# Optimization experiments

Hardware: AMD Instinct MI355X
Metric: run time of the kernel (lower is better)

The kernel has to match this reference:

```python
import jax, jax.numpy as jnp
import numpy as np

D_MODEL = 1024
D_STATE = 64


def setup_inputs() -> dict:
    key = jax.random.key(0)
    k_x, k_a, k_b, k_c, k_d = jax.random.split(key, 5)
    x = jax.random.normal(k_x, (4, 4096, D_MODEL), dtype=jnp.float32)
    # parameter init mirrors _init_parameters
    A_diag = jax.random.uniform(k_a, (D_STATE,), minval=-0.5, maxval=0.5, dtype=jnp.float32)
    def xavier(k, shape):
        fan_in, fan_out = shape
        limit = float(np.sqrt(6.0 / (fan_in + fan_out)))
        return jax.random.uniform(k, shape, minval=-limit, maxval=limit, dtype=jnp.float32)
    B = xavier(k_b, (D_MODEL, D_STATE))
    C = xavier(k_c, (D_STATE, D_MODEL))
    D = xavier(k_d, (D_MODEL, D_MODEL)) * 0.1
    return {"x": x, "A_diag": A_diag, "B": B, "C": C, "D": D}


def reference(x, A_diag, B, C, D):
    # h_t = sigmoid(A_diag) * h_{t-1} + x_t @ B ; y_t = h_t @ C + x_t @ D
    # dropout is identity in eval mode.
    a = jax.nn.sigmoid(A_diag)                      # [S_state]
    u = jnp.einsum('btd,ds->bts', x, B)             # precompute input drive [B,T,S]

    def step(h, u_t):                               # h: [B,S], u_t: [B,S]
        h = a * h + u_t
        return h, h

    h0 = jnp.zeros((x.shape[0], A_diag.shape[0]), dtype=x.dtype)
    _, hs = jax.lax.scan(step, h0, jnp.swapaxes(u, 0, 1))  # hs: [T,B,S]
    hs = jnp.swapaxes(hs, 0, 1)                            # [B,T,S]
    y = jnp.einsum('bts,sd->btd', hs, C) + jnp.einsum('btd,de->bte', x, D)
    return y
```

## Files before the change

kernel.cpp:

```cpp
#include <hip/hip_runtime.h>
#include <hip/hip_bf16.h>

using bf16x8 = __attribute__((ext_vector_type(8))) __bf16;
using f32x4  = __attribute__((ext_vector_type(4))) float;
using f32x16 = __attribute__((ext_vector_type(16))) float;

#define MTOT   16384
#define DMODEL 1024
#define DSTATE 64
#define KBIG   1088

__device__ __forceinline__ ushort f2b(float f) {
  __hip_bfloat16 h = __float2bfloat16(f);
  return *reinterpret_cast<ushort*>(&h);
}

__device__ __forceinline__ void gld_lds16(const ushort* g, const char* l) {
  using gptr_t = const __attribute__((address_space(1))) uint32_t*;
  using lptr_t = __attribute__((address_space(3))) uint32_t*;
  __builtin_amdgcn_global_load_lds(
      reinterpret_cast<gptr_t>(reinterpret_cast<uintptr_t>(g)),
      reinterpret_cast<lptr_t>(static_cast<uint32_t>(reinterpret_cast<uintptr_t>(l))),
      16, 0, 0);
}

#define BARRIER() do { asm volatile("" ::: "memory"); __builtin_amdgcn_s_barrier(); asm volatile("" ::: "memory"); } while (0)
#define VMCNT8() asm volatile("s_waitcnt vmcnt(8)" ::: "memory")
#define VMCNT0() asm volatile("s_waitcnt vmcnt(0)" ::: "memory")

__global__ void prep_params(const float* __restrict__ A_diag, const float* __restrict__ B,
                            const float* __restrict__ C, const float* __restrict__ D,
                            ushort* __restrict__ Wt, ushort* __restrict__ Btu,
                            float* __restrict__ aSig) {
  int i = blockIdx.x * blockDim.x + threadIdx.x;
  int stride = gridDim.x * blockDim.x;
  for (int idx = i; idx < DMODEL * KBIG; idx += stride) {
    int n = idx / KBIG, k = idx % KBIG;
    float v = (k < DSTATE) ? C[k * DMODEL + n] : D[(size_t)(k - DSTATE) * DMODEL + n];
    Wt[idx] = f2b(v);
  }
  for (int idx = i; idx < DSTATE * DMODEL; idx += stride) {
    int s = idx >> 10, k = idx & 1023;
    Btu[idx] = f2b(B[k * DSTATE + s]);
  }
  if (i < DSTATE) aSig[i] = 1.0f / (1.0f + expf(-A_diag[i]));
}

__global__ __launch_bounds__(256) void fused_xu(const float* __restrict__ x,
    const ushort* __restrict__ Btu, const float* __restrict__ aSig,
    ushort* __restrict__ Z, float* __restrict__ Uloc, float* __restrict__ carry) {
  __shared__ ushort As[64][136];
  __shared__ float  Ul[64][68];
  int tid = threadIdx.x;
  int w = tid >> 6, lane = tid & 63;
  int l16 = lane & 15, lh = lane >> 4;
  int row0 = blockIdx.x * 64;

  f32x4 acc[4] = {};
  float4 xv[4][2];
#pragma unroll
  for (int p = 0; p < 4; ++p) {
    int fi = p * 256 + tid;
    int r = fi >> 4, kq = fi & 15;
    const float* src = x + (size_t)(row0 + r) * 1024 + kq * 8;
    xv[p][0] = *reinterpret_cast<const float4*>(src);
    xv[p][1] = *reinterpret_cast<const float4*>(src + 4);
  }
  for (int c = 0; c < 8; ++c) {
    int k0 = c * 128;
#pragma unroll
    for (int p = 0; p < 4; ++p) {
      int fi = p * 256 + tid;
      int r = fi >> 4, kq = fi & 15;
      ushort o[8] = {f2b(xv[p][0].x), f2b(xv[p][0].y), f2b(xv[p][0].z), f2b(xv[p][0].w),
                     f2b(xv[p][1].x), f2b(xv[p][1].y), f2b(xv[p][1].z), f2b(xv[p][1].w)};
      uint4 pk = *reinterpret_cast<uint4*>(o);
      *reinterpret_cast<uint4*>(&Z[(size_t)(row0 + r) * KBIG + DSTATE + k0 + kq * 8]) = pk;
      *reinterpret_cast<uint4*>(&As[r][kq * 8]) = pk;
    }
    __syncthreads();
    if (c < 7) {
      int k1 = k0 + 128;
#pragma unroll
      for (int p = 0; p < 4; ++p) {
        int fi = p * 256 + tid;
        int r = fi >> 4, kq = fi & 15;
        const float* src = x + (size_t)(row0 + r) * 1024 + k1 + kq * 8;
        xv[p][0] = *reinterpret_cast<const float4*>(src);
        xv[p][1] = *reinterpret_cast<const float4*>(src + 4);
      }
    }
#pragma unroll
    for (int ks = 0; ks < 4; ++ks) {
      bf16x8 af = *reinterpret_cast<const bf16x8*>(&As[w * 16 + l16][ks * 32 + lh * 8]);
#pragma unroll
      for (int n = 0; n < 4; ++n) {
        bf16x8 bf = *reinterpret_cast<const bf16x8*>(
            &Btu[(size_t)(n * 16 + l16) * 1024 + k0 + ks * 32 + lh * 8]);
        acc[n] = __builtin_amdgcn_mfma_f32_16x16x32_bf16(af, bf, acc[n], 0, 0, 0);
      }
    }
    __syncthreads();
  }
#pragma unroll
  for (int n = 0; n < 4; ++n)
#pragma unroll
    for (int j = 0; j < 4; ++j)
      Ul[w * 16 + lh * 4 + j][n * 16 + l16] = acc[n][j];
  __syncthreads();
  int s = lane;
  float as = aSig[s];
  float h = 0.0f;
  int g = blockIdx.x * 4 + w;
#pragma unroll
  for (int i = 0; i < 16; ++i) {
    h = fmaf(as, h, Ul[w * 16 + i][s]);
    Uloc[(size_t)(g * 16 + i) * 64 + s] = h;
  }
  carry[(size_t)g * 64 + s] = h;
}

__global__ __launch_bounds__(256) void scan_fix2(const float* __restrict__ aSig,
    const float* __restrict__ Uloc, const float* __restrict__ carry,
    ushort* __restrict__ Z) {
  int w = threadIdx.x >> 6, s = threadIdx.x & 63;
  int g = blockIdx.x * 4 + w;
  int b = g >> 8, c = g & 255;
  float as = aSig[s];
  float aL = as;
#pragma unroll
  for (int q = 0; q < 4; ++q) aL *= aL;
  const float* cb = carry + ((size_t)b << 8) * 64 + s;
  float H = 0.0f;
  for (int c0 = 0; c0 < 256; c0 += 16) {
    if (c0 >= c) break;
    float v[16];
#pragma unroll
    for (int i = 0; i < 16; ++i) v[i] = cb[(size_t)(c0 + i) * 64];
#pragma unroll
    for (int i = 0; i < 16; ++i)
      if (c0 + i < c) H = fmaf(aL, H, v[i]);
  }
  float p = as;
  size_t ubase = (size_t)g * 16 * 64 + s;
  size_t zbase = (size_t)(g * 16) * KBIG + s;
#pragma unroll
  for (int i = 0; i < 16; ++i) {
    float h = fmaf(p, H, Uloc[ubase + (size_t)i * 64]);
    p *= as;
    Z[zbase + (size_t)i * KBIG] = f2b(h);
  }
}

__global__ __launch_bounds__(512) void gemm256(const ushort* __restrict__ A, int lda,
                                               const ushort* __restrict__ Bt, int ldb,
                                               float* __restrict__ Cc, int ldc, int K) {
  extern __shared__ __align__(128) char smem[];
  const int tid = threadIdx.x;
  const int wid = tid >> 6, lane = tid & 63;
  const int wm = wid >> 2, wn = wid & 3;
  const int l32 = lane & 31, kh = lane >> 5;

  int bid = blockIdx.x;
  int swz = (bid & 7) * ((int)gridDim.x >> 3) + (bid >> 3);
  const int bmRow = (swz >> 2) * 256;
  const int bnCol = (swz & 3) * 256;
  const int NT = K / 64;

  const int sRow = lane >> 3;
  const int sCol = (((lane & 7) ^ (lane >> 3)) << 3);

  const ushort* aBase = A + (size_t)(bmRow + wid * 8 + sRow) * lda + sCol;
  const ushort* bBase = Bt + (size_t)(bnCol + wid * 8 + sRow) * ldb + sCol;
  char* aDst0 = smem + (wid * 8) * 128;
  char* bDst0 = smem + 32768 + (wid * 8) * 128;

  const int aRB = (wm * 128 + l32) * 128 + ((kh ^ (l32 & 7)) << 4);
  const int bRB = 32768 + (wn * 64 + l32) * 128 + ((kh ^ (l32 & 7)) << 4);

  f32x16 acc[4][2] = {};
  bf16x8 aC[4], bC[2], aN[4], bN[2];

  auto stageA = [&](int buf, int t, int h) {
    const ushort* g0 = aBase + (size_t)(h * 128) * lda + (size_t)t * 64;
    const char* d = aDst0 + buf + h * 128 * 128;
    gld_lds16(g0, d);
    gld_lds16(g0 + (size_t)64 * lda, d + 64 * 128);
  };
  auto stageB = [&](int buf, int t, int h) {
    const ushort* g0 = bBase + (size_t)(h * 128) * ldb + (size_t)t * 64;
    const char* d = bDst0 + buf + h * 128 * 128;
    gld_lds16(g0, d);
    gld_lds16(g0 + (size_t)64 * ldb, d + 64 * 128);
  };
  auto readA = [&](bf16x8 (&d)[4], int buf, int ks) {
#pragma unroll
    for (int mb = 0; mb < 4; ++mb)
      d[mb] = *reinterpret_cast<const bf16x8*>(smem + buf + ((aRB + mb * 4096) ^ (ks << 5)));
  };
  auto readB = [&](bf16x8 (&d)[2], int buf, int ks) {
#pragma unroll
    for (int qn = 0; qn < 2; ++qn)
      d[qn] = *reinterpret_cast<const bf16x8*>(smem + buf + ((bRB + qn * 4096) ^ (ks << 5)));
  };
  auto mfmaC = [&](bf16x8 (&a4)[4], bf16x8 (&b2)[2]) {
    __builtin_amdgcn_s_setprio(1);
#pragma unroll
    for (int mb = 0; mb < 4; ++mb)
#pragma unroll
      for (int qn = 0; qn < 2; ++qn)
        acc[mb][qn] = __builtin_amdgcn_mfma_f32_32x32x16_bf16(
            a4[mb], b2[qn], acc[mb][qn], 0, 0, 0);
    __builtin_amdgcn_s_setprio(0);
  };

  stageA(0, 0, 0); stageA(0, 0, 1); stageB(0, 0, 0); stageB(0, 0, 1);
  stageA(65536, 1, 0); stageA(65536, 1, 1); stageB(65536, 1, 0); stageB(65536, 1, 1);
  VMCNT8();
  BARRIER();
  readA(aC, 0, 0); readB(bC, 0, 0);

  for (int t = 0; t < NT; ++t) {
    const int buf = (t & 1) << 16;
    const bool st2 = (t + 2 < NT);
    const bool nxt = (t + 1 < NT);
    readA(aN, buf, 1); readB(bN, buf, 1);
    mfmaC(aC, bC);
    readA(aC, buf, 2); readB(bC, buf, 2);
    mfmaC(aN, bN);
    readA(aN, buf, 3); readB(bN, buf, 3);
    mfmaC(aC, bC);
    BARRIER();
    if (st2) {
      stageA(buf, t + 2, 0); stageA(buf, t + 2, 1);
      stageB(buf, t + 2, 0); stageB(buf, t + 2, 1);
      VMCNT8();
    } else {
      VMCNT0();
    }
    BARRIER();
    if (nxt) { readA(aC, buf ^ 65536, 0); readB(bC, buf ^ 65536, 0); }
    mfmaC(aN, bN);
  }

#pragma unroll
  for (int mb = 0; mb < 4; ++mb)
#pragma unroll
    for (int qn = 0; qn < 2; ++qn)
#pragma unroll
      for (int reg = 0; reg < 16; ++reg) {
        int r = bmRow + wm * 128 + mb * 32 + (reg & 3) + 8 * (reg >> 2) + 4 * kh;
        int c = bnCol + wn * 64 + qn * 32 + l32;
        Cc[(size_t)r * ldc + c] = acc[mb][qn][reg];
      }
}

extern "C" void kernel_launch(void* const* d_in, const int* in_sizes, int n_in,
                              void* d_out, int out_size, void* d_ws, size_t ws_size,
                              hipStream_t stream) {
  const float* x      = (const float*)d_in[0];
  const float* A_diag = (const float*)d_in[1];
  const float* B      = (const float*)d_in[2];
  const float* C      = (const float*)d_in[3];
  const float* D      = (const float*)d_in[4];
  float* y = (float*)d_out;

  char* w = (char*)d_ws;
  ushort* Z     = (ushort*)(w);
  ushort* Wt    = (ushort*)(w + 35651584);
  ushort* Btu   = (ushort*)(w + 37879808);
  float*  Uloc  = (float*) (w + 38010880);
  float*  carry = (float*) (w + 42205184);
  float*  aSig  = (float*) (w + 42467328);

  (void)hipFuncSetAttribute(reinterpret_cast<const void*>(&gemm256),
                            hipFuncAttributeMaxDynamicSharedMemorySize, 131072);

  prep_params<<<dim3(1024), dim3(256), 0, stream>>>(A_diag, B, C, D, Wt, Btu, aSig);
  fused_xu<<<dim3(256), dim3(256), 0, stream>>>(x, Btu, aSig, Z, Uloc, carry);
  scan_fix2<<<dim3(256), dim3(256), 0, stream>>>(aSig, Uloc, carry, Z);
  gemm256<<<dim3(64 * 4), dim3(512), 131072, stream>>>(Z, KBIG, Wt, KBIG, y, DMODEL, KBIG);
}
```

Baseline: 89.01 us.

## Restructure GEMM to 128x256 tiles with 16x16 MFMA and direct global B loads

Rewrites the main GEMM so each block computes a 128x256 tile, which doubles the grid to 512 blocks. Only the A operand is staged through LDS, double-buffered. The B operand is read straight from global memory into registers each K-step, and the 32x32x16 MFMA is replaced by 16x16x32. The aim is more blocks per CU and less LDS traffic. In exchange, B is re-read from global/L2 by every block with no LDS reuse, and each step waits on a full vmcnt(0) that exposes load latency.

```diff
diff --git a/kernel.cpp b/kernel.cpp
--- a/kernel.cpp
+++ b/kernel.cpp
@@ -3,7 +3,6 @@
 
 using bf16x8 = __attribute__((ext_vector_type(8))) __bf16;
 using f32x4  = __attribute__((ext_vector_type(4))) float;
-using f32x16 = __attribute__((ext_vector_type(16))) float;
 
 #define MTOT   16384
 #define DMODEL 1024
@@ -25,7 +24,6 @@
 }
 
 #define BARRIER() do { asm volatile("" ::: "memory"); __builtin_amdgcn_s_barrier(); asm volatile("" ::: "memory"); } while (0)
-#define VMCNT8() asm volatile("s_waitcnt vmcnt(8)" ::: "memory")
 #define VMCNT0() asm volatile("s_waitcnt vmcnt(0)" ::: "memory")
 
 __global__ void prep_params(const float* __restrict__ A_diag, const float* __restrict__ B,
@@ -159,99 +157,76 @@
   const int tid = threadIdx.x;
   const int wid = tid >> 6, lane = tid & 63;
   const int wm = wid >> 2, wn = wid & 3;
-  const int l32 = lane & 31, kh = lane >> 5;
+  const int l16 = lane & 15, lh = lane >> 4;
 
   int bid = blockIdx.x;
   int swz = (bid & 7) * ((int)gridDim.x >> 3) + (bid >> 3);
-  const int bmRow = (swz >> 2) * 256;
+  const int bmRow = (swz >> 2) * 128;
   const int bnCol = (swz & 3) * 256;
   const int NT = K / 64;
 
+  const int cswz = ((lh ^ (l16 & 7)) << 4);
   const int sRow = lane >> 3;
   const int sCol = (((lane & 7) ^ (lane >> 3)) << 3);
 
-  const ushort* aBase = A + (size_t)(bmRow + wid * 8 + sRow) * lda + sCol;
-  const ushort* bBase = Bt + (size_t)(bnCol + wid * 8 + sRow) * ldb + sCol;
-  char* aDst0 = smem + (wid * 8) * 128;
-  char* bDst0 = smem + 32768 + (wid * 8) * 128;
-
-  const int aRB = (wm * 128 + l32) * 128 + ((kh ^ (l32 & 7)) << 4);
-  const int bRB = 32768 + (wn * 64 + l32) * 128 + ((kh ^ (l32 & 7)) << 4);
-
-  f32x16 acc[4][2] = {};
-  bf16x8 aC[4], bC[2], aN[4], bN[2];
-
-  auto stageA = [&](int buf, int t, int h) {
-    const ushort* g0 = aBase + (size_t)(h * 128) * lda + (size_t)t * 64;
-    const char* d = aDst0 + buf + h * 128 * 128;
-    gld_lds16(g0, d);
-    gld_lds16(g0 + (size_t)64 * lda, d + 64 * 128);
-  };
-  auto stageB = [&](int buf, int t, int h) {
-    const ushort* g0 = bBase + (size_t)(h * 128) * ldb + (size_t)t * 64;
-    const char* d = bDst0 + buf + h * 128 * 128;
-    gld_lds16(g0, d);
-    gld_lds16(g0 + (size_t)64 * ldb, d + 64 * 128);
-  };
-  auto readA = [&](bf16x8 (&d)[4], int buf, int ks) {
-#pragma unroll
-    for (int mb = 0; mb < 4; ++mb)
-      d[mb] = *reinterpret_cast<const bf16x8*>(smem + buf + ((aRB + mb * 4096) ^ (ks << 5)));
-  };
-  auto readB = [&](bf16x8 (&d)[2], int buf, int ks) {
-#pragma unroll
-    for (int qn = 0; qn < 2; ++qn)
-      d[qn] = *reinterpret_cast<const bf16x8*>(smem + buf + ((bRB + qn * 4096) ^ (ks << 5)));
-  };
-  auto mfmaC = [&](bf16x8 (&a4)[4], bf16x8 (&b2)[2]) {
+  const ushort* aBase = A + (size_t)(bmRow + wid * 16 + sRow) * lda + sCol;
+  char* aDst = smem + (wid * 16) * 128;
+
+  f32x4 acc[4][4] = {};
+  bf16x8 aC[4], aN[4], bC[4], bN[4];
+
+  auto stageA = [&](int buf, int t) {
+    const ushort* g = aBase + (size_t)t * 64;
+    char* d = aDst + buf;
+    gld_lds16(g, d);
+    gld_lds16(g + (size_t)8 * lda, d + 8 * 128);
+  };
+  auto readA = [&](bf16x8 (&dst)[4], int buf, int ks) {
+#pragma unroll
+    for (int m = 0; m < 4; ++m)
+      dst[m] = *reinterpret_cast<const bf16x8*>(
+          smem + buf + (wm * 64 + m * 16 + l16) * 128 + (cswz ^ (ks << 6)));
+  };
+  auto loadB = [&](bf16x8 (&dst)[4], int t, int ks) {
+#pragma unroll
+    for (int n = 0; n < 4; ++n)
+      dst[n] = *reinterpret_cast<const bf16x8*>(
+          Bt + (size_t)(bnCol + wn * 64 + n * 16 + l16) * ldb + t * 64 + ks * 32 + lh * 8);
+  };
+  auto mfmaK = [&](bf16x8 (&a4)[4], bf16x8 (&b4)[4]) {
     __builtin_amdgcn_s_setprio(1);
 #pragma unroll
-    for (int mb = 0; mb < 4; ++mb)
-#pragma unroll
-      for (int qn = 0; qn < 2; ++qn)
-        acc[mb][qn] = __builtin_amdgcn_mfma_f32_32x32x16_bf16(
-            a4[mb], b2[qn], acc[mb][qn], 0, 0, 0);
+    for (int m = 0; m < 4; ++m)
+#pragma unroll
+      for (int n = 0; n < 4; ++n)
+        acc[m][n] = __builtin_amdgcn_mfma_f32_16x16x32_bf16(a4[m], b4[n], acc[m][n], 0, 0, 0);
     __builtin_amdgcn_s_setprio(0);
   };
 
-  stageA(0, 0, 0); stageA(0, 0, 1); stageB(0, 0, 0); stageB(0, 0, 1);
-  stageA(65536, 1, 0); stageA(65536, 1, 1); stageB(65536, 1, 0); stageB(65536, 1, 1);
-  VMCNT8();
+  stageA(0, 0);
+  VMCNT0();
   BARRIER();
-  readA(aC, 0, 0); readB(bC, 0, 0);
 
   for (int t = 0; t < NT; ++t) {
-    const int buf = (t & 1) << 16;
-    const bool st2 = (t + 2 < NT);
-    const bool nxt = (t + 1 < NT);
-    readA(aN, buf, 1); readB(bN, buf, 1);
-    mfmaC(aC, bC);
-    readA(aC, buf, 2); readB(bC, buf, 2);
-    mfmaC(aN, bN);
-    readA(aN, buf, 3); readB(bN, buf, 3);
-    mfmaC(aC, bC);
+    const int buf = (t & 1) << 14;
+    if (t + 1 < NT) stageA(buf ^ 16384, t + 1);
+    loadB(bC, t, 0); loadB(bN, t, 1);
+    readA(aC, buf, 0); readA(aN, buf, 1);
+    mfmaK(aC, bC);
+    mfmaK(aN, bN);
+    VMCNT0();
     BARRIER();
-    if (st2) {
-      stageA(buf, t + 2, 0); stageA(buf, t + 2, 1);
-      stageB(buf, t + 2, 0); stageB(buf, t + 2, 1);
-      VMCNT8();
-    } else {
-      VMCNT0();
-    }
-    BARRIER();
-    if (nxt) { readA(aC, buf ^ 65536, 0); readB(bC, buf ^ 65536, 0); }
-    mfmaC(aN, bN);
-  }
-
-#pragma unroll
-  for (int mb = 0; mb < 4; ++mb)
-#pragma unroll
-    for (int qn = 0; qn < 2; ++qn)
-#pragma unroll
-      for (int reg = 0; reg < 16; ++reg) {
-        int r = bmRow + wm * 128 + mb * 32 + (reg & 3) + 8 * (reg >> 2) + 4 * kh;
-        int c = bnCol + wn * 64 + qn * 32 + l32;
-        Cc[(size_t)r * ldc + c] = acc[mb][qn][reg];
+  }
+
+#pragma unroll
+  for (int m = 0; m < 4; ++m)
+#pragma unroll
+    for (int n = 0; n < 4; ++n)
+#pragma unroll
+      for (int j = 0; j < 4; ++j) {
+        int r = bmRow + wm * 64 + m * 16 + lh * 4 + j;
+        int c = bnCol + wn * 64 + n * 16 + l16;
+        Cc[(size_t)r * ldc + c] = acc[m][n][j];
       }
 }
 
@@ -274,10 +249,10 @@
   float*  aSig  = (float*) (w + 42467328);
 
   (void)hipFuncSetAttribute(reinterpret_cast<const void*>(&gemm256),
-                            hipFuncAttributeMaxDynamicSharedMemorySize, 131072);
+                            hipFuncAttributeMaxDynamicSharedMemorySize, 65536);
 
   prep_params<<<dim3(1024), dim3(256), 0, stream>>>(A_diag, B, C, D, Wt, Btu, aSig);
   fused_xu<<<dim3(256), dim3(256), 0, stream>>>(x, Btu, aSig, Z, Uloc, carry);
   scan_fix2<<<dim3(256), dim3(256), 0, stream>>>(aSig, Uloc, carry, Z);
-  gemm256<<<dim3(64 * 4), dim3(512), 131072, stream>>>(Z, KBIG, Wt, KBIG, y, DMODEL, KBIG);
-}
+  gemm256<<<dim3(128 * 4), dim3(512), 32768, stream>>>(Z, KBIG, Wt, KBIG, y, DMODEL, KBIG);
+}
```

Measured after the change: 142.3 us. +59.9%, slower.
